# Kernel tuning notes

Hardware: AMD Instinct MI355X
Metric: run time of the kernel (lower is better)

## Reference

```python
import jax, jax.numpy as jnp
import numpy as np

B, C, D, H = 2, 1024, 1024, 16
DH = D // H
EPS = 1e-8


def setup_inputs() -> dict:
    key = jax.random.key(0)
    ks = jax.random.split(key, 12)
    s = 0.02
    return {
        "x": jax.random.normal(ks[0], (B, C, D), dtype=jnp.float32),
        "rms_w": jnp.ones((C, D), dtype=jnp.float32),
        "rms_b": jnp.zeros((C, D), dtype=jnp.float32),
        "Wqkv": jax.random.normal(ks[1], (3 * D, D), dtype=jnp.float32) * s,
        "Wout": jax.random.normal(ks[2], (D, D), dtype=jnp.float32) * s,
        "bout": jnp.zeros((D,), dtype=jnp.float32),
        "Wf": jax.random.normal(ks[3], (D, D), dtype=jnp.float32) * s,
        "bf": jnp.zeros((D,), dtype=jnp.float32),
        "Ww": jax.random.normal(ks[4], (D, D), dtype=jnp.float32) * s,
        "bw": jnp.zeros((D,), dtype=jnp.float32),
        "Wv": jax.random.normal(ks[5], (D, D), dtype=jnp.float32) * s,
        "bv": jnp.zeros((D,), dtype=jnp.float32),
        "beta": jnp.ones((1,), dtype=jnp.float32),
    }


def _rope_cos_sin(C, dh):
    # faithful to source: theta = 10000 ** (-2*(i-1)/dh), i in [0, dh//2)
    i = jnp.arange(dh // 2, dtype=jnp.float32)
    theta = 10000.0 ** (-2.0 * (i - 1.0) / dh)            # [dh//2]
    ang = jnp.arange(C, dtype=jnp.float32)[:, None] * theta  # [C, dh//2]
    return jnp.cos(ang), jnp.sin(ang)


def _rotate(t, cos, sin):
    # equivalent to einsum('bhci,cij->bhcj', t, R) with the source R
    ev, od = t[..., 0::2], t[..., 1::2]          # [B,H,C,dh//2]
    out_ev = ev * cos + od * sin
    out_od = -ev * sin + od * cos
    return jnp.stack([out_ev, out_od], axis=-1).reshape(t.shape)


def _rmsnorm(x, w, b):
    rms = jnp.sqrt(jnp.mean(x * x, axis=-1, keepdims=True) + EPS)
    return w * (x / rms) + b


def _attention(x, Wqkv, Wout, bout):
    qkv = x @ Wqkv.T                               # [B,C,3D]
    q, k, v = jnp.split(qkv, 3, axis=-1)
    def heads(t):
        return t.reshape(B, C, H, DH).transpose(0, 2, 1, 3)  # [B,H,C,dh]
    q, k, v = heads(q), heads(k), heads(v)
    cos, sin = _rope_cos_sin(C, DH)
    qr = _rotate(q, cos, sin)
    kr = _rotate(k, cos, sin)
    scale = 1.0 / jnp.sqrt(jnp.float32(DH))
    num = jnp.exp(jnp.einsum('bhid,bhjd->bhij', qr, kr) * scale)
    den = jnp.sum(jnp.exp(jnp.einsum('bhid,bhjd->bhij', q, k) * scale),
                  axis=-1, keepdims=True)
    attn = num / den
    mask = jnp.tril(jnp.ones((C, C), dtype=bool))
    attn = jnp.where(mask[None, None], attn, 0.0)
    y = attn @ v                                   # [B,H,C,dh]
    y = y.transpose(0, 2, 1, 3).reshape(B, C, D)
    return y @ Wout.T + bout


def _ffn(x, Wf, bf, Ww, bw, Wv, bv, beta):
    h = x @ Wf.T + bf
    wx = h @ Ww.T + bw
    swish = wx * jax.nn.sigmoid(beta * wx)
    return swish * (h @ Wv.T + bv)


def reference(x, rms_w, rms_b, Wqkv, Wout, bout, Wf, bf, Ww, bw, Wv, bv, beta):
    # dropout p is identity in eval mode
    x = _rmsnorm(x, rms_w, rms_b)
    x = x + _attention(x, Wqkv, Wout, bout)
    x = _rmsnorm(x, rms_w, rms_b)   # same shared RMSNorm module applied twice
    x = x + _ffn(x, Wf, bf, Ww, bw, Wv, bv, beta)
    return x
```

## Files before the change

kernel.cpp:

```cpp
#include <hip/hip_runtime.h>
#include <math.h>

#define B_ 2
#define C_ 1024
#define D_ 1024
#define H_ 16
#define DH_ 64
#define EPSF 1e-8f
#define BK 32

typedef __bf16 bf16;
typedef __attribute__((ext_vector_type(4))) __bf16 bf16x4;
typedef __attribute__((ext_vector_type(8))) __bf16 bf16x8;
typedef __attribute__((ext_vector_type(4))) float f32x4;

__device__ inline f32x4 mfma16(bf16x8 a, bf16x8 b, f32x4 c) {
  return __builtin_amdgcn_mfma_f32_16x16x32_bf16(a, b, c, 0, 0, 0);
}

__device__ inline void async16(const bf16* g, bf16* l) {
  __builtin_amdgcn_global_load_lds((const __attribute__((address_space(1))) void*)g,
                                   (__attribute__((address_space(3))) void*)l, 16, 0, 0);
}

__global__ __launch_bounds__(256) void cvt_kernel(const float* __restrict__ src,
                                                  bf16* __restrict__ dst) {
  int idx = (blockIdx.x * 256 + threadIdx.x) * 4;
  float4 v = *(const float4*)(src + idx);
  bf16x4 o;
  o[0] = (bf16)v.x; o[1] = (bf16)v.y; o[2] = (bf16)v.z; o[3] = (bf16)v.w;
  *(bf16x4*)(dst + idx) = o;
}

__global__ __launch_bounds__(256) void cvt4_kernel(const float* __restrict__ s0,
                                                   const float* __restrict__ s1,
                                                   const float* __restrict__ s2,
                                                   const float* __restrict__ s3,
                                                   bf16* __restrict__ dst) {
  int which = blockIdx.x >> 10;
  int local = (blockIdx.x & 1023) * 1024 + threadIdx.x * 4;
  const float* src = which == 0 ? s0 : which == 1 ? s1 : which == 2 ? s2 : s3;
  float4 v = *(const float4*)(src + local);
  bf16x4 o;
  o[0] = (bf16)v.x; o[1] = (bf16)v.y; o[2] = (bf16)v.z; o[3] = (bf16)v.w;
  *(bf16x4*)(dst + (size_t)which * (D_ * D_) + local) = o;
}

__global__ __launch_bounds__(256) void rmsnorm_f32_kernel(const float* __restrict__ x,
                                                          const float* __restrict__ w,
                                                          const float* __restrict__ b,
                                                          bf16* __restrict__ out) {
  int row = blockIdx.x;
  int c = row & (C_ - 1);
  int t = threadIdx.x;
  float4 xv = *(const float4*)(x + (size_t)row * D_ + t * 4);
  float ss = xv.x * xv.x + xv.y * xv.y + xv.z * xv.z + xv.w * xv.w;
#pragma unroll
  for (int m = 1; m < 64; m <<= 1) ss += __shfl_xor(ss, m, 64);
  __shared__ float red[4];
  if ((t & 63) == 0) red[t >> 6] = ss;
  __syncthreads();
  float tot = red[0] + red[1] + red[2] + red[3];
  float inv = rsqrtf(tot * (1.0f / D_) + EPSF);
  float4 wv = *(const float4*)(w + (size_t)c * D_ + t * 4);
  float4 bv = *(const float4*)(b + (size_t)c * D_ + t * 4);
  bf16x4 ov;
  ov[0] = (bf16)(wv.x * (xv.x * inv) + bv.x);
  ov[1] = (bf16)(wv.y * (xv.y * inv) + bv.y);
  ov[2] = (bf16)(wv.z * (xv.z * inv) + bv.z);
  ov[3] = (bf16)(wv.w * (xv.w * inv) + bv.w);
  *(bf16x4*)(out + (size_t)row * D_ + t * 4) = ov;
}

__global__ __launch_bounds__(256) void rmsnorm_bf16_kernel(const bf16* __restrict__ x,
                                                           const float* __restrict__ w,
                                                           const float* __restrict__ b,
                                                           bf16* __restrict__ out) {
  int row = blockIdx.x;
  int c = row & (C_ - 1);
  int t = threadIdx.x;
  bf16x4 xv = *(const bf16x4*)(x + (size_t)row * D_ + t * 4);
  float f0 = (float)xv[0], f1 = (float)xv[1], f2 = (float)xv[2], f3 = (float)xv[3];
  float ss = f0 * f0 + f1 * f1 + f2 * f2 + f3 * f3;
#pragma unroll
  for (int m = 1; m < 64; m <<= 1) ss += __shfl_xor(ss, m, 64);
  __shared__ float red[4];
  if ((t & 63) == 0) red[t >> 6] = ss;
  __syncthreads();
  float tot = red[0] + red[1] + red[2] + red[3];
  float inv = rsqrtf(tot * (1.0f / D_) + EPSF);
  float4 wv = *(const float4*)(w + (size_t)c * D_ + t * 4);
  float4 bv = *(const float4*)(b + (size_t)c * D_ + t * 4);
  bf16x4 ov;
  ov[0] = (bf16)(wv.x * (f0 * inv) + bv.x);
  ov[1] = (bf16)(wv.y * (f1 * inv) + bv.y);
  ov[2] = (bf16)(wv.z * (f2 * inv) + bv.z);
  ov[3] = (bf16)(wv.w * (f3 * inv) + bv.w);
  *(bf16x4*)(out + (size_t)row * D_ + t * 4) = ov;
}

template <int BMt, int BNt, bool DUAL>
__global__ __launch_bounds__(256) void gemm_lds(const bf16* __restrict__ A,
                                                const bf16* __restrict__ W1,
                                                const bf16* __restrict__ W2,
                                                const float* __restrict__ b1,
                                                const float* __restrict__ b2,
                                                const bf16* __restrict__ R,
                                                bf16* __restrict__ O1,
                                                bf16* __restrict__ O2,
                                                int M, int N1, int K) {
  constexpr int MT = BMt / 32;
  constexpr int NT = BNt / 32;
  __shared__ bf16 sa[BMt * BK];
  __shared__ bf16 sb[BNt * BK];
  int t = threadIdx.x, l = t & 63, w = t >> 6;
  int m0 = blockIdx.y * BMt;
  int n0g = blockIdx.x * BNt;
  const bf16* W = (!DUAL || n0g < N1) ? W1 : W2;
  const float* bias = (!DUAL || n0g < N1) ? b1 : b2;
  bf16* Cout = (!DUAL || n0g < N1) ? O1 : O2;
  int n0 = DUAL ? (n0g & (N1 - 1)) : n0g;
  int wm = (w >> 1) * (BMt / 2), wn = (w & 1) * (BNt / 2);
  int lm = l & 15, lq = l >> 4;
  f32x4 acc[MT][NT] = {};

  for (int k0 = 0; k0 < K; k0 += BK) {
    __syncthreads();
#pragma unroll
    for (int p = 0; p < BMt / 64; ++p) {
      int lin = p * 256 + t;
      async16(A + (size_t)(m0 + (lin >> 2)) * K + k0 + (lin & 3) * 8, sa + lin * 8);
    }
#pragma unroll
    for (int p = 0; p < BNt / 64; ++p) {
      int lin = p * 256 + t;
      async16(W + (size_t)(n0 + (lin >> 2)) * K + k0 + (lin & 3) * 8, sb + lin * 8);
    }
    __syncthreads();
    bf16x8 af[MT], bfr[NT];
#pragma unroll
    for (int mt = 0; mt < MT; ++mt)
      af[mt] = *(const bf16x8*)(sa + (wm + mt * 16 + lm) * BK + lq * 8);
#pragma unroll
    for (int nt = 0; nt < NT; ++nt)
      bfr[nt] = *(const bf16x8*)(sb + (wn + nt * 16 + lm) * BK + lq * 8);
#pragma unroll
    for (int mt = 0; mt < MT; ++mt)
#pragma unroll
      for (int nt = 0; nt < NT; ++nt)
        acc[mt][nt] = mfma16(af[mt], bfr[nt], acc[mt][nt]);
  }
#pragma unroll
  for (int mt = 0; mt < MT; ++mt)
#pragma unroll
    for (int nt = 0; nt < NT; ++nt) {
      int col = n0 + wn + nt * 16 + lm;
      float bb = bias ? bias[col] : 0.0f;
#pragma unroll
      for (int r = 0; r < 4; ++r) {
        int row = m0 + wm + mt * 16 + lq * 4 + r;
        float v = acc[mt][nt][r] + bb;
        if (R) v += (float)R[(size_t)row * N1 + col];
        Cout[(size_t)row * N1 + col] = (bf16)v;
      }
    }
}

__global__ __launch_bounds__(256) void prep_kernel(const bf16* __restrict__ qkv,
                                                   bf16* __restrict__ qr,
                                                   bf16* __restrict__ kr,
                                                   bf16* __restrict__ vt) {
  __shared__ bf16 tile[64][65];
  int t = threadIdx.x;
  int blk = blockIdx.x;
  int ct = blk & 15;
  int h = (blk >> 4) & 15;
  int b = blk >> 8;
  int c0 = ct * 64;
  size_t hb = (size_t)((b * H_ + h) * C_);

#pragma unroll
  for (int p = 0; p < 2; ++p) {
    int row = p * 32 + (t >> 3);
    int col = (t & 7) * 8;
    int c = c0 + row;
    size_t gq = (size_t)(b * C_ + c) * (3 * D_) + h * DH_ + col;
    bf16x8 qv = *(const bf16x8*)(qkv + gq);
    bf16x8 kv = *(const bf16x8*)(qkv + gq + D_);
    bf16x8 qo, ko;
#pragma unroll
    for (int j = 0; j < 4; ++j) {
      int i = (col >> 1) + j;
      float theta = exp2f(-13.287712379549449f * (2.0f * ((float)i - 1.0f) / 64.0f));
      float ang = (float)c * theta;
      float sv = __sinf(ang), cv = __cosf(ang);
      float qe = (float)qv[2 * j], qo_ = (float)qv[2 * j + 1];
      float ke = (float)kv[2 * j], ko_ = (float)kv[2 * j + 1];
      qo[2 * j] = (bf16)(qe * cv + qo_ * sv);
      qo[2 * j + 1] = (bf16)(qo_ * cv - qe * sv);
      ko[2 * j] = (bf16)(ke * cv + ko_ * sv);
      ko[2 * j + 1] = (bf16)(ko_ * cv - ke * sv);
    }
    *(bf16x8*)(qr + (hb + c) * DH_ + col) = qo;
    *(bf16x8*)(kr + (hb + c) * DH_ + col) = ko;
  }

#pragma unroll
  for (int p = 0; p < 16; ++p) {
    int lin = p * 256 + t;
    int cl = lin >> 6, dh = lin & 63;
    tile[dh][cl] = qkv[(size_t)(b * C_ + c0 + cl) * (3 * D_) + 2 * D_ + h * DH_ + dh];
  }
  __syncthreads();
  size_t vbase = (size_t)((b * H_ + h) * DH_) * C_;
#pragma unroll
  for (int p = 0; p < 16; ++p) {
    int lin = p * 256 + t;
    int dh = lin >> 6, cl = lin & 63;
    vt[vbase + (size_t)dh * C_ + c0 + cl] = tile[dh][cl];
  }
}

__global__ __launch_bounds__(256) void attn_kernel(const bf16* __restrict__ qkv,
                                                   const bf16* __restrict__ qr,
                                                   const bf16* __restrict__ kr,
                                                   const bf16* __restrict__ vt,
                                                   bf16* __restrict__ y) {
  __shared__ bf16 sk[64 * 72];
  __shared__ bf16 skr[64 * 72];
  __shared__ bf16 sv[64 * 72];
  __shared__ bf16 pl[4][16 * 72];
  int t = threadIdx.x, l = t & 63, w = t >> 6;
  int blk = blockIdx.x;
  int it = blk & 15;
  int h = (blk >> 4) & 15;
  int b = blk >> 8;
  int i_base = it * 64 + w * 16;
  int lm = l & 15, lq = l >> 4;
  const float scale = 0.125f;

  size_t hq = (size_t)h * DH_;
  size_t qrow = (size_t)(b * C_ + i_base + lm) * (3 * D_) + hq;
  size_t hb = (size_t)((b * H_ + h) * C_);
  bf16x8 qp[2], qrf[2];
#pragma unroll
  for (int kk = 0; kk < 2; ++kk) {
    qp[kk] = *(const bf16x8*)(qkv + qrow + kk * 32 + lq * 8);
    qrf[kk] = *(const bf16x8*)(qr + (hb + i_base + lm) * DH_ + kk * 32 + lq * 8);
  }

  float den[4] = {0.f, 0.f, 0.f, 0.f};
  f32x4 yacc[4] = {};
  int i_max = i_base + 15;
  size_t kbase = (size_t)(b * C_) * (3 * D_) + D_ + hq;
  size_t krbase = hb * DH_;
  size_t vtbase = (size_t)((b * H_ + h) * DH_) * C_;
  int sr = t >> 3;
  int sc = (t & 7) * 8;

  int4 pk0, pk1, pkr0, pkr1, pv0, pv1;
#define FETCH_TILE(J0)                                                               \
  pk0 = *(const int4*)(qkv + kbase + (size_t)((J0) + sr) * (3 * D_) + sc);           \
  pk1 = *(const int4*)(qkv + kbase + (size_t)((J0) + 32 + sr) * (3 * D_) + sc);      \
  pkr0 = *(const int4*)(kr + krbase + (size_t)((J0) + sr) * DH_ + sc);               \
  pkr1 = *(const int4*)(kr + krbase + (size_t)((J0) + 32 + sr) * DH_ + sc);          \
  pv0 = *(const int4*)(vt + vtbase + (size_t)sr * C_ + (J0) + sc);                   \
  pv1 = *(const int4*)(vt + vtbase + (size_t)(32 + sr) * C_ + (J0) + sc);

  FETCH_TILE(0)

  for (int j0 = 0; j0 < C_; j0 += 64) {
    __syncthreads();
    *(int4*)(sk + sr * 72 + sc) = pk0;
    *(int4*)(sk + (32 + sr) * 72 + sc) = pk1;
    *(int4*)(skr + sr * 72 + sc) = pkr0;
    *(int4*)(skr + (32 + sr) * 72 + sc) = pkr1;
    *(int4*)(sv + sr * 72 + sc) = pv0;
    *(int4*)(sv + (32 + sr) * 72 + sc) = pv1;
    __syncthreads();
    if (j0 + 64 < C_) {
      FETCH_TILE(j0 + 64)
    }
#pragma unroll
    for (int js = 0; js < 64; js += 16) {
      bf16x8 kf0 = *(const bf16x8*)(sk + (js + lm) * 72 + lq * 8);
      bf16x8 kf1 = *(const bf16x8*)(sk + (js + lm) * 72 + 32 + lq * 8);
      f32x4 s = {0.f, 0.f, 0.f, 0.f};
      s = mfma16(qp[0], kf0, s);
      s = mfma16(qp[1], kf1, s);
#pragma unroll
      for (int r = 0; r < 4; ++r) den[r] += __expf(s[r] * scale);
    }
    if (j0 <= i_max) {
#pragma unroll
      for (int js = 0; js < 64; js += 16) {
        bf16x8 kf0 = *(const bf16x8*)(skr + (js + lm) * 72 + lq * 8);
        bf16x8 kf1 = *(const bf16x8*)(skr + (js + lm) * 72 + 32 + lq * 8);
        f32x4 s = {0.f, 0.f, 0.f, 0.f};
        s = mfma16(qrf[0], kf0, s);
        s = mfma16(qrf[1], kf1, s);
#pragma unroll
        for (int r = 0; r < 4; ++r) {
          int jg = j0 + js + lm;
          int ig = i_base + lq * 4 + r;
          float p = (jg <= ig) ? __expf(s[r] * scale) : 0.0f;
          pl[w][(lq * 4 + r) * 72 + js + lm] = (bf16)p;
        }
      }
      __builtin_amdgcn_wave_barrier();
      bf16x8 pf0 = *(const bf16x8*)(pl[w] + lm * 72 + lq * 8);
      bf16x8 pf1 = *(const bf16x8*)(pl[w] + lm * 72 + 32 + lq * 8);
#pragma unroll
      for (int tt = 0; tt < 4; ++tt) {
        bf16x8 vf0 = *(const bf16x8*)(sv + (tt * 16 + lm) * 72 + lq * 8);
        bf16x8 vf1 = *(const bf16x8*)(sv + (tt * 16 + lm) * 72 + 32 + lq * 8);
        yacc[tt] = mfma16(pf0, vf0, mfma16(pf1, vf1, yacc[tt]));
      }
      __builtin_amdgcn_wave_barrier();
    }
  }
#undef FETCH_TILE
  float inv[4];
#pragma unroll
  for (int r = 0; r < 4; ++r) {
    float d = den[r];
    d += __shfl_xor(d, 1, 64);
    d += __shfl_xor(d, 2, 64);
    d += __shfl_xor(d, 4, 64);
    d += __shfl_xor(d, 8, 64);
    inv[r] = 1.0f / d;
  }
#pragma unroll
  for (int tt = 0; tt < 4; ++tt)
#pragma unroll
    for (int r = 0; r < 4; ++r) {
      int ig = i_base + lq * 4 + r;
      y[(size_t)(b * C_ + ig) * D_ + hq + tt * 16 + lm] = (bf16)(yacc[tt][r] * inv[r]);
    }
}

__global__ __launch_bounds__(256) void ffn_final_kernel(const bf16* __restrict__ x3,
                                                        const bf16* __restrict__ wx,
                                                        const bf16* __restrict__ hv,
                                                        const float* __restrict__ beta_p,
                                                        float* __restrict__ out, int n) {
  int idx = blockIdx.x * 256 + threadIdx.x;
  if (idx >= n) return;
  float beta = beta_p[0];
  float z = (float)wx[idx];
  float sw = z / (1.0f + __expf(-beta * z));
  out[idx] = (float)x3[idx] + sw * (float)hv[idx];
}

extern "C" void kernel_launch(void* const* d_in, const int* in_sizes, int n_in,
                              void* d_out, int out_size, void* d_ws, size_t ws_size,
                              hipStream_t stream) {
  const float* x = (const float*)d_in[0];
  const float* rms_w = (const float*)d_in[1];
  const float* rms_b = (const float*)d_in[2];
  const float* Wqkv = (const float*)d_in[3];
  const float* Wout = (const float*)d_in[4];
  const float* bout = (const float*)d_in[5];
  const float* Wf = (const float*)d_in[6];
  const float* bfp = (const float*)d_in[7];
  const float* Ww = (const float*)d_in[8];
  const float* bw = (const float*)d_in[9];
  const float* Wv = (const float*)d_in[10];
  const float* bv = (const float*)d_in[11];
  const float* beta = (const float*)d_in[12];
  float* out = (float*)d_out;

  bf16* ws = (bf16*)d_ws;
  const size_t MC = (size_t)B_ * C_;
  const size_t M1 = MC * D_;
  bf16* x1 = ws + 0 * M1;
  bf16* qkv = ws + 1 * M1;
  bf16* qr = ws + 4 * M1;
  bf16* kr = ws + 5 * M1;
  bf16* vt = ws + 6 * M1;
  bf16* y = (bf16*)d_out;
  bf16* Wqkv_bf = ws + 4 * M1;
  bf16* W4 = ws + 1 * M1;
  bf16* x2 = ws + 4 * M1;
  bf16* x3 = ws + 5 * M1;
  bf16* hbuf = ws + 6 * M1;
  bf16* wx = ws + 3 * M1;
  bf16* hv = ws + 0 * M1;

  rmsnorm_f32_kernel<<<MC, 256, 0, stream>>>(x, rms_w, rms_b, x1);
  cvt_kernel<<<(3 * D_ * D_) / 1024, 256, 0, stream>>>(Wqkv, Wqkv_bf);
  gemm_lds<128, 64, false><<<dim3(3 * D_ / 64, MC / 128), 256, 0, stream>>>(
      x1, Wqkv_bf, nullptr, nullptr, nullptr, nullptr, qkv, nullptr, MC, 3 * D_, D_);
  prep_kernel<<<B_ * H_ * (C_ / 64), 256, 0, stream>>>(qkv, qr, kr, vt);
  attn_kernel<<<B_ * H_ * (C_ / 64), 256, 0, stream>>>(qkv, qr, kr, vt, y);
  cvt4_kernel<<<4 * (D_ * D_) / 1024, 256, 0, stream>>>(Wout, Wf, Ww, Wv, W4);
  gemm_lds<64, 64, false><<<dim3(D_ / 64, MC / 64), 256, 0, stream>>>(
      y, W4, nullptr, bout, nullptr, x1, x2, nullptr, MC, D_, D_);
  rmsnorm_bf16_kernel<<<MC, 256, 0, stream>>>(x2, rms_w, rms_b, x3);
  gemm_lds<64, 64, false><<<dim3(D_ / 64, MC / 64), 256, 0, stream>>>(
      x3, W4 + (size_t)(D_ * D_), nullptr, bfp, nullptr, nullptr, hbuf, nullptr, MC, D_, D_);
  gemm_lds<64, 64, true><<<dim3(2 * D_ / 64, MC / 64), 256, 0, stream>>>(
      hbuf, W4 + 2 * (size_t)(D_ * D_), W4 + 3 * (size_t)(D_ * D_), bw, bv, nullptr, wx, hv,
      MC, D_, D_);
  ffn_final_kernel<<<(int)((MC * D_) / 256), 256, 0, stream>>>(x3, wx, hv, beta, out,
                                                               (int)(MC * D_));
}
```

Measured before the change: 234.8 us.

## Split attention over key halves, fuse FFN gate epilogue, merge weight conversions

Attention now runs twice as many blocks, each covering half of the key range. The blocks write fp32 partial outputs and denominators, and a new combine kernel sums and normalises them, giving more parallelism on the long sequential key loop. The dual Ww/Wv GEMM now computes both products in one block and applies the swish gate and residual in its epilogue, which removes the separate elementwise kernel and the bf16 intermediate buffers. All weight conversions are merged into one launch. The cost is extra fp32 partial traffic, an extra combine launch, and a larger workspace.

New measurement: 233.8 us. About the same (-0.4%).

```diff
diff --git a/kernel.cpp b/kernel.cpp
--- a/kernel.cpp
+++ b/kernel.cpp
@@ -23,27 +23,20 @@
                                    (__attribute__((address_space(3))) void*)l, 16, 0, 0);
 }
 
-__global__ __launch_bounds__(256) void cvt_kernel(const float* __restrict__ src,
-                                                  bf16* __restrict__ dst) {
-  int idx = (blockIdx.x * 256 + threadIdx.x) * 4;
-  float4 v = *(const float4*)(src + idx);
-  bf16x4 o;
-  o[0] = (bf16)v.x; o[1] = (bf16)v.y; o[2] = (bf16)v.z; o[3] = (bf16)v.w;
-  *(bf16x4*)(dst + idx) = o;
-}
-
-__global__ __launch_bounds__(256) void cvt4_kernel(const float* __restrict__ s0,
-                                                   const float* __restrict__ s1,
-                                                   const float* __restrict__ s2,
-                                                   const float* __restrict__ s3,
-                                                   bf16* __restrict__ dst) {
-  int which = blockIdx.x >> 10;
+__global__ __launch_bounds__(256) void cvt_all_kernel(const float* __restrict__ wqkv,
+                                                      const float* __restrict__ wout,
+                                                      const float* __restrict__ wf,
+                                                      const float* __restrict__ www,
+                                                      const float* __restrict__ wv,
+                                                      bf16* __restrict__ dst) {
+  int seg = blockIdx.x >> 10;
   int local = (blockIdx.x & 1023) * 1024 + threadIdx.x * 4;
-  const float* src = which == 0 ? s0 : which == 1 ? s1 : which == 2 ? s2 : s3;
+  const float* src = seg < 3 ? wqkv + (size_t)seg * (D_ * D_)
+                   : seg == 3 ? wout : seg == 4 ? wf : seg == 5 ? www : wv;
   float4 v = *(const float4*)(src + local);
   bf16x4 o;
   o[0] = (bf16)v.x; o[1] = (bf16)v.y; o[2] = (bf16)v.z; o[3] = (bf16)v.w;
-  *(bf16x4*)(dst + (size_t)which * (D_ * D_) + local) = o;
+  *(bf16x4*)(dst + (size_t)seg * (D_ * D_) + local) = o;
 }
 
 __global__ __launch_bounds__(256) void rmsnorm_f32_kernel(const float* __restrict__ x,
@@ -99,27 +92,20 @@
   *(bf16x4*)(out + (size_t)row * D_ + t * 4) = ov;
 }
 
-template <int BMt, int BNt, bool DUAL>
+template <int BMt, int BNt>
 __global__ __launch_bounds__(256) void gemm_lds(const bf16* __restrict__ A,
-                                                const bf16* __restrict__ W1,
-                                                const bf16* __restrict__ W2,
-                                                const float* __restrict__ b1,
-                                                const float* __restrict__ b2,
+                                                const bf16* __restrict__ W,
+                                                const float* __restrict__ bias,
                                                 const bf16* __restrict__ R,
-                                                bf16* __restrict__ O1,
-                                                bf16* __restrict__ O2,
-                                                int M, int N1, int K) {
+                                                bf16* __restrict__ Cout,
+                                                int M, int N, int K) {
   constexpr int MT = BMt / 32;
   constexpr int NT = BNt / 32;
   __shared__ bf16 sa[BMt * BK];
   __shared__ bf16 sb[BNt * BK];
   int t = threadIdx.x, l = t & 63, w = t >> 6;
   int m0 = blockIdx.y * BMt;
-  int n0g = blockIdx.x * BNt;
-  const bf16* W = (!DUAL || n0g < N1) ? W1 : W2;
-  const float* bias = (!DUAL || n0g < N1) ? b1 : b2;
-  bf16* Cout = (!DUAL || n0g < N1) ? O1 : O2;
-  int n0 = DUAL ? (n0g & (N1 - 1)) : n0g;
+  int n0 = blockIdx.x * BNt;
   int wm = (w >> 1) * (BMt / 2), wn = (w & 1) * (BNt / 2);
   int lm = l & 15, lq = l >> 4;
   f32x4 acc[MT][NT] = {};
@@ -160,8 +146,66 @@
       for (int r = 0; r < 4; ++r) {
         int row = m0 + wm + mt * 16 + lq * 4 + r;
         float v = acc[mt][nt][r] + bb;
-        if (R) v += (float)R[(size_t)row * N1 + col];
-        Cout[(size_t)row * N1 + col] = (bf16)v;
+        if (R) v += (float)R[(size_t)row * N + col];
+        Cout[(size_t)row * N + col] = (bf16)v;
+      }
+    }
+}
+
+__global__ __launch_bounds__(256) void gemm_ffn_kernel(const bf16* __restrict__ A,
+                                                       const bf16* __restrict__ Ww,
+                                                       const bf16* __restrict__ Wv,
+                                                       const float* __restrict__ bw,
+                                                       const float* __restrict__ bv,
+                                                       const bf16* __restrict__ x3,
+                                                       const float* __restrict__ beta_p,
+                                                       float* __restrict__ out) {
+  __shared__ bf16 sa[64 * BK];
+  __shared__ bf16 sb1[64 * BK];
+  __shared__ bf16 sb2[64 * BK];
+  int t = threadIdx.x, l = t & 63, w = t >> 6;
+  int m0 = blockIdx.y * 64, n0 = blockIdx.x * 64;
+  int wm = (w >> 1) * 32, wn = (w & 1) * 32;
+  int lm = l & 15, lq = l >> 4;
+  float beta = beta_p[0];
+  f32x4 acc1[2][2] = {}, acc2[2][2] = {};
+
+  for (int k0 = 0; k0 < D_; k0 += BK) {
+    __syncthreads();
+    async16(A + (size_t)(m0 + (t >> 2)) * D_ + k0 + (t & 3) * 8, sa + t * 8);
+    async16(Ww + (size_t)(n0 + (t >> 2)) * D_ + k0 + (t & 3) * 8, sb1 + t * 8);
+    async16(Wv + (size_t)(n0 + (t >> 2)) * D_ + k0 + (t & 3) * 8, sb2 + t * 8);
+    __syncthreads();
+    bf16x8 af[2], b1f[2], b2f[2];
+#pragma unroll
+    for (int mt = 0; mt < 2; ++mt)
+      af[mt] = *(const bf16x8*)(sa + (wm + mt * 16 + lm) * BK + lq * 8);
+#pragma unroll
+    for (int nt = 0; nt < 2; ++nt) {
+      b1f[nt] = *(const bf16x8*)(sb1 + (wn + nt * 16 + lm) * BK + lq * 8);
+      b2f[nt] = *(const bf16x8*)(sb2 + (wn + nt * 16 + lm) * BK + lq * 8);
+    }
+#pragma unroll
+    for (int mt = 0; mt < 2; ++mt)
+#pragma unroll
+      for (int nt = 0; nt < 2; ++nt) {
+        acc1[mt][nt] = mfma16(af[mt], b1f[nt], acc1[mt][nt]);
+        acc2[mt][nt] = mfma16(af[mt], b2f[nt], acc2[mt][nt]);
+      }
+  }
+#pragma unroll
+  for (int mt = 0; mt < 2; ++mt)
+#pragma unroll
+    for (int nt = 0; nt < 2; ++nt) {
+      int col = n0 + wn + nt * 16 + lm;
+      float bbw = bw[col], bbv = bv[col];
+#pragma unroll
+      for (int r = 0; r < 4; ++r) {
+        int row = m0 + wm + mt * 16 + lq * 4 + r;
+        float z = acc1[mt][nt][r] + bbw;
+        float g = acc2[mt][nt][r] + bbv;
+        float sw = z / (1.0f + __expf(-beta * z));
+        out[(size_t)row * D_ + col] = (float)x3[(size_t)row * D_ + col] + sw * g;
       }
     }
 }
@@ -225,19 +269,22 @@
                                                    const bf16* __restrict__ qr,
                                                    const bf16* __restrict__ kr,
                                                    const bf16* __restrict__ vt,
-                                                   bf16* __restrict__ y) {
+                                                   float* __restrict__ yp,
+                                                   float* __restrict__ dp) {
   __shared__ bf16 sk[64 * 72];
   __shared__ bf16 skr[64 * 72];
   __shared__ bf16 sv[64 * 72];
   __shared__ bf16 pl[4][16 * 72];
   int t = threadIdx.x, l = t & 63, w = t >> 6;
   int blk = blockIdx.x;
-  int it = blk & 15;
-  int h = (blk >> 4) & 15;
-  int b = blk >> 8;
+  int half = blk & 1;
+  int it = (blk >> 1) & 15;
+  int h = (blk >> 5) & 15;
+  int b = blk >> 9;
   int i_base = it * 64 + w * 16;
   int lm = l & 15, lq = l >> 4;
   const float scale = 0.125f;
+  int jf = half << 9;
 
   size_t hq = (size_t)h * DH_;
   size_t qrow = (size_t)(b * C_ + i_base + lm) * (3 * D_) + hq;
@@ -267,9 +314,9 @@
   pv0 = *(const int4*)(vt + vtbase + (size_t)sr * C_ + (J0) + sc);                   \
   pv1 = *(const int4*)(vt + vtbase + (size_t)(32 + sr) * C_ + (J0) + sc);
 
-  FETCH_TILE(0)
-
-  for (int j0 = 0; j0 < C_; j0 += 64) {
+  FETCH_TILE(jf)
+
+  for (int j0 = jf; j0 < jf + 512; j0 += 64) {
     __syncthreads();
     *(int4*)(sk + sr * 72 + sc) = pk0;
     *(int4*)(sk + (32 + sr) * 72 + sc) = pk1;
@@ -278,7 +325,7 @@
     *(int4*)(sv + sr * 72 + sc) = pv0;
     *(int4*)(sv + (32 + sr) * 72 + sc) = pv1;
     __syncthreads();
-    if (j0 + 64 < C_) {
+    if (j0 + 64 < jf + 512) {
       FETCH_TILE(j0 + 64)
     }
 #pragma unroll
@@ -320,7 +367,6 @@
     }
   }
 #undef FETCH_TILE
-  float inv[4];
 #pragma unroll
   for (int r = 0; r < 4; ++r) {
     float d = den[r];
@@ -328,28 +374,37 @@
     d += __shfl_xor(d, 2, 64);
     d += __shfl_xor(d, 4, 64);
     d += __shfl_xor(d, 8, 64);
-    inv[r] = 1.0f / d;
-  }
+    if (lm == 0) dp[(size_t)blk * 64 + w * 16 + lq * 4 + r] = d;
+  }
+  size_t yb = (size_t)blk * 4096;
 #pragma unroll
   for (int tt = 0; tt < 4; ++tt)
 #pragma unroll
-    for (int r = 0; r < 4; ++r) {
-      int ig = i_base + lq * 4 + r;
-      y[(size_t)(b * C_ + ig) * D_ + hq + tt * 16 + lm] = (bf16)(yacc[tt][r] * inv[r]);
-    }
-}
-
-__global__ __launch_bounds__(256) void ffn_final_kernel(const bf16* __restrict__ x3,
-                                                        const bf16* __restrict__ wx,
-                                                        const bf16* __restrict__ hv,
-                                                        const float* __restrict__ beta_p,
-                                                        float* __restrict__ out, int n) {
-  int idx = blockIdx.x * 256 + threadIdx.x;
-  if (idx >= n) return;
-  float beta = beta_p[0];
-  float z = (float)wx[idx];
-  float sw = z / (1.0f + __expf(-beta * z));
-  out[idx] = (float)x3[idx] + sw * (float)hv[idx];
+    for (int r = 0; r < 4; ++r)
+      yp[yb + (size_t)(w * 16 + lq * 4 + r) * 64 + tt * 16 + lm] = yacc[tt][r];
+}
+
+__global__ __launch_bounds__(256) void combine_kernel(const float* __restrict__ yp,
+                                                      const float* __restrict__ dp,
+                                                      bf16* __restrict__ y) {
+  int cb = blockIdx.x;
+  int it = cb & 15;
+  int h = (cb >> 4) & 15;
+  int b = cb >> 8;
+  int t = threadIdx.x;
+  int row = t >> 2;
+  int cg = (t & 3) * 16;
+  size_t p0 = (size_t)(cb * 2) * 4096 + (size_t)row * 64 + cg;
+  size_t p1 = p0 + 4096;
+  float inv = 1.0f / (dp[(size_t)(cb * 2) * 64 + row] + dp[(size_t)(cb * 2 + 1) * 64 + row]);
+  bf16x8 o0, o1;
+#pragma unroll
+  for (int c = 0; c < 8; ++c) o0[c] = (bf16)((yp[p0 + c] + yp[p1 + c]) * inv);
+#pragma unroll
+  for (int c = 0; c < 8; ++c) o1[c] = (bf16)((yp[p0 + 8 + c] + yp[p1 + 8 + c]) * inv);
+  size_t ob = (size_t)(b * C_ + it * 64 + row) * D_ + h * DH_ + cg;
+  *(bf16x8*)(y + ob) = o0;
+  *(bf16x8*)(y + ob + 8) = o1;
 }
 
 extern "C" void kernel_launch(void* const* d_in, const int* in_sizes, int n_in,
@@ -371,37 +426,33 @@
   float* out = (float*)d_out;
 
   bf16* ws = (bf16*)d_ws;
+  const size_t DD = (size_t)D_ * D_;
   const size_t MC = (size_t)B_ * C_;
-  const size_t M1 = MC * D_;
-  bf16* x1 = ws + 0 * M1;
-  bf16* qkv = ws + 1 * M1;
-  bf16* qr = ws + 4 * M1;
-  bf16* kr = ws + 5 * M1;
-  bf16* vt = ws + 6 * M1;
+  bf16* wb = ws;
+  bf16* x1 = ws + 7 * DD;
+  bf16* qkv = ws + 9 * DD;
+  bf16* qr = ws + 15 * DD;
+  bf16* kr = ws + 17 * DD;
+  bf16* vt = ws + 19 * DD;
+  bf16* x2 = ws + 21 * DD;
+  bf16* x3 = ws + 23 * DD;
+  bf16* hbuf = ws + 25 * DD;
+  float* yp = (float*)(ws + 28 * DD);
+  float* dp = yp + (size_t)1024 * 4096;
   bf16* y = (bf16*)d_out;
-  bf16* Wqkv_bf = ws + 4 * M1;
-  bf16* W4 = ws + 1 * M1;
-  bf16* x2 = ws + 4 * M1;
-  bf16* x3 = ws + 5 * M1;
-  bf16* hbuf = ws + 6 * M1;
-  bf16* wx = ws + 3 * M1;
-  bf16* hv = ws + 0 * M1;
-
+
+  cvt_all_kernel<<<7 * 1024, 256, 0, stream>>>(Wqkv, Wout, Wf, Ww, Wv, wb);
   rmsnorm_f32_kernel<<<MC, 256, 0, stream>>>(x, rms_w, rms_b, x1);
-  cvt_kernel<<<(3 * D_ * D_) / 1024, 256, 0, stream>>>(Wqkv, Wqkv_bf);
-  gemm_lds<128, 64, false><<<dim3(3 * D_ / 64, MC / 128), 256, 0, stream>>>(
-      x1, Wqkv_bf, nullptr, nullptr, nullptr, nullptr, qkv, nullptr, MC, 3 * D_, D_);
+  gemm_lds<128, 64><<<dim3(3 * D_ / 64, MC / 128), 256, 0, stream>>>(
+      x1, wb, nullptr, nullptr, qkv, MC, 3 * D_, D_);
   prep_kernel<<<B_ * H_ * (C_ / 64), 256, 0, stream>>>(qkv, qr, kr, vt);
-  attn_kernel<<<B_ * H_ * (C_ / 64), 256, 0, stream>>>(qkv, qr, kr, vt, y);
-  cvt4_kernel<<<4 * (D_ * D_) / 1024, 256, 0, stream>>>(Wout, Wf, Ww, Wv, W4);
-  gemm_lds<64, 64, false><<<dim3(D_ / 64, MC / 64), 256, 0, stream>>>(
-      y, W4, nullptr, bout, nullptr, x1, x2, nullptr, MC, D_, D_);
+  attn_kernel<<<B_ * H_ * 16 * 2, 256, 0, stream>>>(qkv, qr, kr, vt, yp, dp);
+  combine_kernel<<<B_ * H_ * 16, 256, 0, stream>>>(yp, dp, y);
+  gemm_lds<64, 64><<<dim3(D_ / 64, MC / 64), 256, 0, stream>>>(
+      y, wb + 3 * DD, bout, x1, x2, MC, D_, D_);
   rmsnorm_bf16_kernel<<<MC, 256, 0, stream>>>(x2, rms_w, rms_b, x3);
-  gemm_lds<64, 64, false><<<dim3(D_ / 64, MC / 64), 256, 0, stream>>>(
-      x3, W4 + (size_t)(D_ * D_), nullptr, bfp, nullptr, nullptr, hbuf, nullptr, MC, D_, D_);
-  gemm_lds<64, 64, true><<<dim3(2 * D_ / 64, MC / 64), 256, 0, stream>>>(
-      hbuf, W4 + 2 * (size_t)(D_ * D_), W4 + 3 * (size_t)(D_ * D_), bw, bv, nullptr, wx, hv,
-      MC, D_, D_);
-  ffn_final_kernel<<<(int)((MC * D_) / 256), 256, 0, stream>>>(x3, wx, hv, beta, out,
-                                                               (int)(MC * D_));
-}
+  gemm_lds<64, 64><<<dim3(D_ / 64, MC / 64), 256, 0, stream>>>(
+      x3, wb + 4 * DD, bfp, nullptr, hbuf, MC, D_, D_);
+  gemm_ffn_kernel<<<dim3(D_ / 64, MC / 64), 256, 0, stream>>>(
+      hbuf, wb + 5 * DD, wb + 6 * DD, bw, bv, x3, beta, out);
+}
```
